# Optimization experiments

Hardware: AMD Instinct MI355X
Metric: run time of the kernel (lower is better)

## Reference

```python
import jax, jax.numpy as jnp
import numpy as np

D_MODEL = 1024
NUM_HEADS = 16
HEAD_DIM = D_MODEL // NUM_HEADS
B, SX, SKV = 4, 2048, 2048


def setup_inputs() -> dict:
    key = jax.random.key(0)
    ks = jax.random.split(key, 6)
    scale = 1.0 / np.sqrt(D_MODEL)
    x = jax.random.normal(ks[0], (B, SX, D_MODEL), dtype=jnp.float32)
    kv = jax.random.normal(ks[1], (B, SKV, D_MODEL), dtype=jnp.float32)
    Wq = jax.random.normal(ks[2], (D_MODEL, D_MODEL), dtype=jnp.float32) * scale
    Wk = jax.random.normal(ks[3], (D_MODEL, D_MODEL), dtype=jnp.float32) * scale
    Wv = jax.random.normal(ks[4], (D_MODEL, D_MODEL), dtype=jnp.float32) * scale
    Wo = jax.random.normal(ks[5], (D_MODEL, D_MODEL), dtype=jnp.float32) * scale
    # causal mask: positions where mask == 0 are filled with -inf
    mask = jnp.tril(jnp.ones((SX, SKV), dtype=jnp.int32))[None, None, :, :]
    return {"x": x, "kv": kv, "mask": mask, "Wq": Wq, "Wk": Wk, "Wv": Wv, "Wo": Wo}


def reference(x, kv, mask, Wq, Wk, Wv, Wo):
    # nn.Linear(bias=False): y = x @ W.T
    q = jnp.einsum('bsd,ed->bse', x, Wq)
    k = jnp.einsum('bsd,ed->bse', kv, Wk)
    v = jnp.einsum('bsd,ed->bse', kv, Wv)
    # split heads -> (B, H, S, hd)
    q = q.reshape(B, SX, NUM_HEADS, HEAD_DIM).transpose(0, 2, 1, 3)
    k = k.reshape(B, SKV, NUM_HEADS, HEAD_DIM).transpose(0, 2, 1, 3)
    v = v.reshape(B, SKV, NUM_HEADS, HEAD_DIM).transpose(0, 2, 1, 3)
    scores = jnp.einsum('bhqd,bhkd->bhqk', q, k) / jnp.sqrt(
        jnp.asarray(HEAD_DIM, dtype=q.dtype))
    scores = jnp.where(mask == 0, -jnp.inf, scores)
    attn = jax.nn.softmax(scores, axis=-1)  # dropout p=0.0 -> identity
    context = jnp.einsum('bhqk,bhkd->bhqd', attn, v)
    context = context.transpose(0, 2, 1, 3).reshape(B, SX, D_MODEL)
    return jnp.einsum('bsd,ed->bse', context, Wo)
```

## Files before the change

kernel.cpp:

```cpp
#include <hip/hip_runtime.h>
#include <hip/hip_bf16.h>
#include <math.h>

#define DM   1024
#define SEQ  2048
#define NH   16
#define HD   64
#define BATCH 4

#define QSCALE 0.180336879f

typedef __attribute__((ext_vector_type(8))) short bf16x8;
typedef __attribute__((ext_vector_type(4))) short short4v;
typedef __attribute__((ext_vector_type(4))) float f32x4;
typedef __attribute__((ext_vector_type(4))) float float4v;

static __device__ inline short f2bf(float f) {
  union { float f; unsigned u; } v; v.f = f;
  unsigned u = v.u + 0x7fff + ((v.u >> 16) & 1);
  return (short)(u >> 16);
}

static __device__ __forceinline__ void async16(const void* g, void* l) {
  __builtin_amdgcn_global_load_lds(
      (const __attribute__((address_space(1))) void*)g,
      (__attribute__((address_space(3))) void*)l, 16, 0, 0);
}

__global__ void conv_all(const float* __restrict__ x, const float* __restrict__ kv,
                         const float* __restrict__ Wq, const float* __restrict__ Wk,
                         const float* __restrict__ Wv, const float* __restrict__ Wo,
                         short* __restrict__ xh, short* __restrict__ kvh,
                         short* __restrict__ Wqh, short* __restrict__ Wkh,
                         short* __restrict__ Wvh, short* __restrict__ Woh)
{
  const int blk = blockIdx.x;
  const float* src; short* hi; int base;
  if (blk < 8192)       { src = x;  hi = xh;  base = blk; }
  else if (blk < 16384) { src = kv; hi = kvh; base = blk - 8192; }
  else {
    int wi = (blk - 16384) >> 10; base = (blk - 16384) & 1023;
    src = wi == 0 ? Wq : wi == 1 ? Wk : wi == 2 ? Wv : Wo;
    hi  = wi == 0 ? Wqh : wi == 1 ? Wkh : wi == 2 ? Wvh : Woh;
  }
  int i = base * 1024 + threadIdx.x * 4;
  float4v v = *(const float4v*)(src + i);
  short4v h;
#pragma unroll
  for (int j = 0; j < 4; j++) h[j] = f2bf(v[j]);
  *(short4v*)(hi + i) = h;
}

template<int OUTMODE>
__global__ __launch_bounds__(256, 2)
void gemm_bt(const short* __restrict__ A, const short* __restrict__ Bh,
             void* __restrict__ C1p, float scale)
{
  __shared__ short As[128 * 32];
  __shared__ short Bs[128 * 32];

  const int t = threadIdx.x;
  const int lane = t & 63, w = t >> 6;
  const int r15 = lane & 15, quad = lane >> 4;
  const int m0 = blockIdx.y * 128, n0 = blockIdx.x * 128;
  const int wm = (w & 1) * 64, wn = (w >> 1) * 64;

  f32x4 acc[4][4];
#pragma unroll
  for (int i = 0; i < 4; i++)
#pragma unroll
    for (int j = 0; j < 4; j++) acc[i][j] = (f32x4)0.0f;

  const int srow = t >> 2, spart = t & 3;
  const int spg = spart ^ (srow & 3);

  for (int k0 = 0; k0 < DM; k0 += 32) {
    size_t ga = (size_t)(m0 + srow) * DM + k0 + spg * 8;
    async16(A + ga,           &As[t * 8]);
    async16(A + ga + 64 * DM, &As[2048 + t * 8]);
    size_t gb = (size_t)(n0 + srow) * DM + k0 + spg * 8;
    async16(Bh + gb,           &Bs[t * 8]);
    async16(Bh + gb + 64 * DM, &Bs[2048 + t * 8]);
    __syncthreads();

    bf16x8 ah[4], bh[4];
#pragma unroll
    for (int mt = 0; mt < 4; mt++) {
      int off = (wm + mt * 16 + r15) * 32 + ((quad * 8) ^ ((r15 & 3) * 8));
      ah[mt] = *(const bf16x8*)&As[off];
    }
#pragma unroll
    for (int nt = 0; nt < 4; nt++) {
      int off = (wn + nt * 16 + r15) * 32 + ((quad * 8) ^ ((r15 & 3) * 8));
      bh[nt] = *(const bf16x8*)&Bs[off];
    }
#pragma unroll
    for (int mt = 0; mt < 4; mt++)
#pragma unroll
      for (int nt = 0; nt < 4; nt++)
        acc[mt][nt] = __builtin_amdgcn_mfma_f32_16x16x32_bf16(ah[mt], bh[nt], acc[mt][nt], 0, 0, 0);
    __syncthreads();
  }

#pragma unroll
  for (int mt = 0; mt < 4; mt++)
#pragma unroll
    for (int nt = 0; nt < 4; nt++)
#pragma unroll
      for (int reg = 0; reg < 4; reg++) {
        int m = m0 + wm + mt * 16 + quad * 4 + reg;
        int n = n0 + wn + nt * 16 + r15;
        float c = acc[mt][nt][reg];
        if (OUTMODE == 1) {
          int s = m & (SEQ - 1), kl = s & 63;
          int sp = (s & ~63) + ((kl & 15) * 4 + (kl >> 4));
          ((short*)C1p)[((size_t)(m >> 11) * DM + n) * SEQ + sp] = f2bf(c);
        } else if (OUTMODE == 2) {
          ((float*)C1p)[(size_t)m * DM + n] = c;
        } else {
          ((short*)C1p)[(size_t)m * DM + n] = f2bf(c * scale);
        }
      }
}

__global__ __launch_bounds__(256, 3)
void attn(const short* __restrict__ Qh_g, const short* __restrict__ Kh_g,
          const short* __restrict__ Vt_g, short* __restrict__ ctx)
{
  __shared__ short KV[2][2 * 4096];
  __shared__ short Plds[4][32][72];

  const int t = threadIdx.x, lane = t & 63, w = t >> 6;
  const int r15 = lane & 15, quad = lane >> 4;
  const int bh = blockIdx.x, b = bh >> 4, h = bh & 15;
  const int qt = 15 - blockIdx.y;
  const int qw = qt * 128 + w * 32;
  const int nkt = 2 * qt + 2;

  const int srow = t >> 3, spg = (t & 7) ^ (srow & 7);
  const int swb = (r15 & 7) * 8;

  const bf16x8 ones = {0x3F80, 0x3F80, 0x3F80, 0x3F80, 0x3F80, 0x3F80, 0x3F80, 0x3F80};

  bf16x8 qh[2][2];
#pragma unroll
  for (int mt = 0; mt < 2; mt++)
#pragma unroll
    for (int ks = 0; ks < 2; ks++)
      qh[mt][ks] = *(const bf16x8*)(Qh_g + (size_t)(b * SEQ + qw + mt * 16 + r15) * DM
                                    + h * HD + ks * 32 + quad * 8);

  f32x4 o[2][4], ol[2];
#pragma unroll
  for (int mt = 0; mt < 2; mt++) {
    ol[mt] = (f32x4)0.0f;
#pragma unroll
    for (int dt = 0; dt < 4; dt++) o[mt][dt] = (f32x4)0.0f;
  }

  auto stage = [&](int kt, int bufi) {
    short* L = &KV[bufi][0];
    size_t kro = (size_t)(b * SEQ + kt * 64 + srow) * DM + h * HD + spg * 8;
    async16(Kh_g + kro,           L + t * 8);
    async16(Kh_g + kro + 32 * DM, L + 2048 + t * 8);
    size_t vro = (size_t)(b * DM + h * HD + srow) * SEQ + kt * 64 + spg * 8;
    async16(Vt_g + vro,            L + 4096 + t * 8);
    async16(Vt_g + vro + 32 * SEQ, L + 6144 + t * 8);
  };

  stage(0, 0);

  for (int kt = 0; kt < nkt; kt++) {
    __syncthreads();
    if (kt + 1 < nkt) stage(kt + 1, (kt + 1) & 1);
    const short* L = &KV[kt & 1][0];
    const int k0 = kt * 64;
    if (k0 > qw + 31) continue;

    f32x4 s[2][4];
#pragma unroll
    for (int nt = 0; nt < 4; nt++) {
      const int kb = k0 + nt * 16;
      if (kb <= qw + 31) {
        const int ro = (nt * 16 + r15) * 64;
        bf16x8 kh0 = *(const bf16x8*)&L[ro + ((quad * 8) ^ swb)];
        bf16x8 kh1 = *(const bf16x8*)&L[ro + (((4 + quad) * 8) ^ swb)];
        f32x4 a1 = (f32x4)0.0f;
        a1 = __builtin_amdgcn_mfma_f32_16x16x32_bf16(qh[1][0], kh0, a1, 0, 0, 0);
        a1 = __builtin_amdgcn_mfma_f32_16x16x32_bf16(qh[1][1], kh1, a1, 0, 0, 0);
        s[1][nt] = a1;
        if (kb <= qw + 15) {
          f32x4 a0 = (f32x4)0.0f;
          a0 = __builtin_amdgcn_mfma_f32_16x16x32_bf16(qh[0][0], kh0, a0, 0, 0, 0);
          a0 = __builtin_amdgcn_mfma_f32_16x16x32_bf16(qh[0][1], kh1, a0, 0, 0, 0);
          s[0][nt] = a0;
        } else {
          s[0][nt] = (f32x4)(-3e38f);
        }
      } else {
        s[0][nt] = (f32x4)(-3e38f);
        s[1][nt] = (f32x4)(-3e38f);
      }
    }

    unsigned up[2][4][2];
    if (k0 + 63 <= qw) {
#pragma unroll
      for (int mt = 0; mt < 2; mt++)
#pragma unroll
        for (int r = 0; r < 4; r++)
#pragma unroll
          for (int nt = 0; nt < 4; nt++) {
            unsigned pu = __float_as_uint(__builtin_amdgcn_exp2f(s[mt][nt][r]));
            if ((nt & 1) == 0) up[mt][r][nt >> 1] = pu >> 16;
            else               up[mt][r][nt >> 1] |= (pu & 0xFFFF0000u);
          }
    } else {
#pragma unroll
      for (int mt = 0; mt < 2; mt++)
#pragma unroll
        for (int r = 0; r < 4; r++) {
          const int qg = qw + mt * 16 + quad * 4 + r;
#pragma unroll
          for (int nt = 0; nt < 4; nt++) {
            float p = __builtin_amdgcn_exp2f(s[mt][nt][r]);
            p = ((k0 + nt * 16 + r15) > qg) ? 0.0f : p;
            unsigned pu = __float_as_uint(p);
            if ((nt & 1) == 0) up[mt][r][nt >> 1] = pu >> 16;
            else               up[mt][r][nt >> 1] |= (pu & 0xFFFF0000u);
          }
        }
    }

#pragma unroll
    for (int mt = 0; mt < 2; mt++)
#pragma unroll
      for (int r = 0; r < 4; r++)
        *(int2*)&Plds[w][mt * 16 + quad * 4 + r][r15 * 4] =
            make_int2((int)up[mt][r][0], (int)up[mt][r][1]);

#pragma unroll
    for (int ks = 0; ks < 2; ks++) {
      bf16x8 pa0 = *(const bf16x8*)&Plds[w][r15][ks * 32 + quad * 8];
      bf16x8 pa1 = *(const bf16x8*)&Plds[w][16 + r15][ks * 32 + quad * 8];
      ol[0] = __builtin_amdgcn_mfma_f32_16x16x32_bf16(pa0, ones, ol[0], 0, 0, 0);
      ol[1] = __builtin_amdgcn_mfma_f32_16x16x32_bf16(pa1, ones, ol[1], 0, 0, 0);
#pragma unroll
      for (int dt = 0; dt < 4; dt++) {
        bf16x8 vb = *(const bf16x8*)&L[4096 + (dt * 16 + r15) * 64 + (((ks * 4 + quad) * 8) ^ swb)];
        o[0][dt] = __builtin_amdgcn_mfma_f32_16x16x32_bf16(pa0, vb, o[0][dt], 0, 0, 0);
        o[1][dt] = __builtin_amdgcn_mfma_f32_16x16x32_bf16(pa1, vb, o[1][dt], 0, 0, 0);
      }
    }
  }

#pragma unroll
  for (int mt = 0; mt < 2; mt++)
#pragma unroll
    for (int r = 0; r < 4; r++) {
      float inv = 1.0f / ol[mt][r];
      int qrow = qw + mt * 16 + quad * 4 + r;
#pragma unroll
      for (int dt = 0; dt < 4; dt++)
        ctx[((size_t)(b * SEQ + qrow)) * DM + h * HD + dt * 16 + r15] =
            f2bf(o[mt][dt][r] * inv);
    }
}

extern "C" void kernel_launch(void* const* d_in, const int* in_sizes, int n_in,
                              void* d_out, int out_size, void* d_ws, size_t ws_size,
                              hipStream_t stream)
{
  const float* x  = (const float*)d_in[0];
  const float* kv = (const float*)d_in[1];
  const float* Wq = (const float*)d_in[3];
  const float* Wk = (const float*)d_in[4];
  const float* Wv = (const float*)d_in[5];
  const float* Wo = (const float*)d_in[6];

  char* ws = (char*)d_ws;
  const size_t SZ  = (size_t)BATCH * SEQ * DM * sizeof(short);
  const size_t WSZ = (size_t)DM * DM * sizeof(short);
  short* xh  = (short*)(ws + 0 * SZ);
  short* kvh = (short*)(ws + 1 * SZ);
  short* Qh  = (short*)(ws + 2 * SZ);
  short* Kh  = (short*)(ws + 3 * SZ);
  short* Vt  = (short*)(ws + 4 * SZ);
  short* ctx = (short*)(ws + 0 * SZ);
  char*  wb  = ws + 5 * SZ;
  short* Wqh = (short*)(wb + 0 * WSZ);
  short* Wkh = (short*)(wb + 1 * WSZ);
  short* Wvh = (short*)(wb + 2 * WSZ);
  short* Woh = (short*)(wb + 3 * WSZ);

  conv_all<<<20480, 256, 0, stream>>>(x, kv, Wq, Wk, Wv, Wo,
                                      xh, kvh, Wqh, Wkh, Wvh, Woh);

  dim3 gg(DM / 128, BATCH * SEQ / 128);
  gemm_bt<3><<<gg, 256, 0, stream>>>(xh,  Wqh, Qh, QSCALE);
  gemm_bt<3><<<gg, 256, 0, stream>>>(kvh, Wkh, Kh, 1.0f);
  gemm_bt<1><<<gg, 256, 0, stream>>>(kvh, Wvh, Vt, 1.0f);

  dim3 ga(NH * BATCH, 16);
  attn<<<ga, 256, 0, stream>>>(Qh, Kh, Vt, ctx);

  gemm_bt<2><<<gg, 256, 0, stream>>>(ctx, Woh, d_out, 1.0f);
}
```

Measured before the change: 300.2 us.

## Double-buffer GEMM K-loop with 64-wide tiles and merge QKV projections into one launch

The GEMM inner loop moves from a single-buffered 32-wide K step to double-buffered 64-wide K tiles. Async global-to-LDS loads for the next tile are issued before the MFMAs on the current tile, and only one barrier is needed per step. The Q, K and V projections are merged into one launch using blockIdx.z, which cuts launch overhead and gives the GPU a larger grid. In exchange, LDS use per block grows to 64KB, which may limit how many blocks fit per CU.

Result: faster. 281.7 us (-6.2%).

```diff
diff --git a/kernel.cpp b/kernel.cpp
--- a/kernel.cpp
+++ b/kernel.cpp
@@ -51,57 +51,130 @@
   *(short4v*)(hi + i) = h;
 }
 
-template<int OUTMODE>
-__global__ __launch_bounds__(256, 2)
-void gemm_bt(const short* __restrict__ A, const short* __restrict__ Bh,
-             void* __restrict__ C1p, float scale)
-{
-  __shared__ short As[128 * 32];
-  __shared__ short Bs[128 * 32];
-
+static __device__ __forceinline__ void gemm_core(
+    const short* __restrict__ A, const short* __restrict__ Bh,
+    short* __restrict__ As, short* __restrict__ Bs,
+    int m0, int n0, f32x4 acc[4][4])
+{
   const int t = threadIdx.x;
   const int lane = t & 63, w = t >> 6;
   const int r15 = lane & 15, quad = lane >> 4;
+  const int wm = (w & 1) * 64, wn = (w >> 1) * 64;
+  const int srow = t >> 3;
+  const int spg = ((t & 7) ^ (srow & 7)) * 8;
+  const int swb = (r15 & 7) * 8;
+
+#pragma unroll
+  for (int i = 0; i < 4; i++)
+#pragma unroll
+    for (int j = 0; j < 4; j++) acc[i][j] = (f32x4)0.0f;
+
+  auto stage = [&](int kt, int bufi) {
+    const int k0 = kt * 64;
+    short* Ad = As + bufi * 8192 + t * 8;
+    short* Bd = Bs + bufi * 8192 + t * 8;
+#pragma unroll
+    for (int i = 0; i < 4; i++) {
+      async16(A  + (size_t)(m0 + srow + 32 * i) * DM + k0 + spg, Ad + i * 2048);
+      async16(Bh + (size_t)(n0 + srow + 32 * i) * DM + k0 + spg, Bd + i * 2048);
+    }
+  };
+
+  stage(0, 0);
+
+  for (int kt = 0; kt < DM / 64; kt++) {
+    __syncthreads();
+    if (kt + 1 < DM / 64) stage(kt + 1, (kt + 1) & 1);
+    const short* Ab = As + (kt & 1) * 8192;
+    const short* Bb = Bs + (kt & 1) * 8192;
+
+    bf16x8 ah[4][2], bh[4][2];
+#pragma unroll
+    for (int mt = 0; mt < 4; mt++) {
+      const int ro = (wm + mt * 16 + r15) * 64;
+#pragma unroll
+      for (int ks = 0; ks < 2; ks++)
+        ah[mt][ks] = *(const bf16x8*)&Ab[ro + (((ks * 4 + quad) * 8) ^ swb)];
+    }
+#pragma unroll
+    for (int nt = 0; nt < 4; nt++) {
+      const int ro = (wn + nt * 16 + r15) * 64;
+#pragma unroll
+      for (int ks = 0; ks < 2; ks++)
+        bh[nt][ks] = *(const bf16x8*)&Bb[ro + (((ks * 4 + quad) * 8) ^ swb)];
+    }
+#pragma unroll
+    for (int mt = 0; mt < 4; mt++)
+#pragma unroll
+      for (int nt = 0; nt < 4; nt++) {
+        acc[mt][nt] = __builtin_amdgcn_mfma_f32_16x16x32_bf16(ah[mt][0], bh[nt][0], acc[mt][nt], 0, 0, 0);
+        acc[mt][nt] = __builtin_amdgcn_mfma_f32_16x16x32_bf16(ah[mt][1], bh[nt][1], acc[mt][nt], 0, 0, 0);
+      }
+  }
+}
+
+__global__ __launch_bounds__(256, 2)
+void gemm_qkv(const short* __restrict__ xh, const short* __restrict__ kvh,
+              const short* __restrict__ Wqh, const short* __restrict__ Wkh,
+              const short* __restrict__ Wvh,
+              short* __restrict__ Qh, short* __restrict__ Kh, short* __restrict__ Vt)
+{
+  __shared__ short As[2][8192];
+  __shared__ short Bs[2][8192];
+  const int z = blockIdx.z;
+  const short* A  = (z == 0) ? xh : kvh;
+  const short* Bm = (z == 0) ? Wqh : (z == 1) ? Wkh : Wvh;
   const int m0 = blockIdx.y * 128, n0 = blockIdx.x * 128;
+
+  f32x4 acc[4][4];
+  gemm_core(A, Bm, &As[0][0], &Bs[0][0], m0, n0, acc);
+
+  const int t = threadIdx.x, lane = t & 63, w = t >> 6;
+  const int r15 = lane & 15, quad = lane >> 4;
   const int wm = (w & 1) * 64, wn = (w >> 1) * 64;
 
+  if (z < 2) {
+    short* Cp = (z == 0) ? Qh : Kh;
+    const float scale = (z == 0) ? QSCALE : 1.0f;
+#pragma unroll
+    for (int mt = 0; mt < 4; mt++)
+#pragma unroll
+      for (int nt = 0; nt < 4; nt++)
+#pragma unroll
+        for (int reg = 0; reg < 4; reg++) {
+          int m = m0 + wm + mt * 16 + quad * 4 + reg;
+          int n = n0 + wn + nt * 16 + r15;
+          Cp[(size_t)m * DM + n] = f2bf(acc[mt][nt][reg] * scale);
+        }
+  } else {
+#pragma unroll
+    for (int mt = 0; mt < 4; mt++)
+#pragma unroll
+      for (int nt = 0; nt < 4; nt++)
+#pragma unroll
+        for (int reg = 0; reg < 4; reg++) {
+          int m = m0 + wm + mt * 16 + quad * 4 + reg;
+          int n = n0 + wn + nt * 16 + r15;
+          int s = m & (SEQ - 1), kl = s & 63;
+          int sp = (s & ~63) + ((kl & 15) * 4 + (kl >> 4));
+          Vt[((size_t)(m >> 11) * DM + n) * SEQ + sp] = f2bf(acc[mt][nt][reg]);
+        }
+  }
+}
+
+__global__ __launch_bounds__(256, 2)
+void gemm_out(const short* __restrict__ ctx, const short* __restrict__ Woh,
+              float* __restrict__ out)
+{
+  __shared__ short As[2][8192];
+  __shared__ short Bs[2][8192];
+  const int m0 = blockIdx.y * 128, n0 = blockIdx.x * 128;
   f32x4 acc[4][4];
-#pragma unroll
-  for (int i = 0; i < 4; i++)
-#pragma unroll
-    for (int j = 0; j < 4; j++) acc[i][j] = (f32x4)0.0f;
-
-  const int srow = t >> 2, spart = t & 3;
-  const int spg = spart ^ (srow & 3);
-
-  for (int k0 = 0; k0 < DM; k0 += 32) {
-    size_t ga = (size_t)(m0 + srow) * DM + k0 + spg * 8;
-    async16(A + ga,           &As[t * 8]);
-    async16(A + ga + 64 * DM, &As[2048 + t * 8]);
-    size_t gb = (size_t)(n0 + srow) * DM + k0 + spg * 8;
-    async16(Bh + gb,           &Bs[t * 8]);
-    async16(Bh + gb + 64 * DM, &Bs[2048 + t * 8]);
-    __syncthreads();
-
-    bf16x8 ah[4], bh[4];
-#pragma unroll
-    for (int mt = 0; mt < 4; mt++) {
-      int off = (wm + mt * 16 + r15) * 32 + ((quad * 8) ^ ((r15 & 3) * 8));
-      ah[mt] = *(const bf16x8*)&As[off];
-    }
-#pragma unroll
-    for (int nt = 0; nt < 4; nt++) {
-      int off = (wn + nt * 16 + r15) * 32 + ((quad * 8) ^ ((r15 & 3) * 8));
-      bh[nt] = *(const bf16x8*)&Bs[off];
-    }
-#pragma unroll
-    for (int mt = 0; mt < 4; mt++)
-#pragma unroll
-      for (int nt = 0; nt < 4; nt++)
-        acc[mt][nt] = __builtin_amdgcn_mfma_f32_16x16x32_bf16(ah[mt], bh[nt], acc[mt][nt], 0, 0, 0);
-    __syncthreads();
-  }
-
+  gemm_core(ctx, Woh, &As[0][0], &Bs[0][0], m0, n0, acc);
+
+  const int t = threadIdx.x, lane = t & 63, w = t >> 6;
+  const int r15 = lane & 15, quad = lane >> 4;
+  const int wm = (w & 1) * 64, wn = (w >> 1) * 64;
 #pragma unroll
   for (int mt = 0; mt < 4; mt++)
 #pragma unroll
@@ -110,16 +183,7 @@
       for (int reg = 0; reg < 4; reg++) {
         int m = m0 + wm + mt * 16 + quad * 4 + reg;
         int n = n0 + wn + nt * 16 + r15;
-        float c = acc[mt][nt][reg];
-        if (OUTMODE == 1) {
-          int s = m & (SEQ - 1), kl = s & 63;
-          int sp = (s & ~63) + ((kl & 15) * 4 + (kl >> 4));
-          ((short*)C1p)[((size_t)(m >> 11) * DM + n) * SEQ + sp] = f2bf(c);
-        } else if (OUTMODE == 2) {
-          ((float*)C1p)[(size_t)m * DM + n] = c;
-        } else {
-          ((short*)C1p)[(size_t)m * DM + n] = f2bf(c * scale);
-        }
+        out[(size_t)m * DM + n] = acc[mt][nt][reg];
       }
 }
 
@@ -296,13 +360,12 @@
   conv_all<<<20480, 256, 0, stream>>>(x, kv, Wq, Wk, Wv, Wo,
                                       xh, kvh, Wqh, Wkh, Wvh, Woh);
 
-  dim3 gg(DM / 128, BATCH * SEQ / 128);
-  gemm_bt<3><<<gg, 256, 0, stream>>>(xh,  Wqh, Qh, QSCALE);
-  gemm_bt<3><<<gg, 256, 0, stream>>>(kvh, Wkh, Kh, 1.0f);
-  gemm_bt<1><<<gg, 256, 0, stream>>>(kvh, Wvh, Vt, 1.0f);
+  dim3 gq(DM / 128, BATCH * SEQ / 128, 3);
+  gemm_qkv<<<gq, 256, 0, stream>>>(xh, kvh, Wqh, Wkh, Wvh, Qh, Kh, Vt);
 
   dim3 ga(NH * BATCH, 16);
   attn<<<ga, 256, 0, stream>>>(Qh, Kh, Vt, ctx);
 
-  gemm_bt<2><<<gg, 256, 0, stream>>>(ctx, Woh, d_out, 1.0f);
-}
+  dim3 gg(DM / 128, BATCH * SEQ / 128);
+  gemm_out<<<gg, 256, 0, stream>>>(ctx, Woh, (float*)d_out);
+}
```
